# Kernel optimization log

Hardware: AMD Instinct MI355X
Metric: run time of the kernel (lower is better)

Reference implementation:

```python
import jax, jax.numpy as jnp
import numpy as np

N = 100000   # num_nodes
E = 1600000  # num_edges (avg degree 16)
F = 128      # input features
U = 128      # units


def setup_inputs() -> dict:
    key = jax.random.key(0)
    k1, k2, k3, k4 = jax.random.split(key, 4)
    x = jax.random.normal(k1, (N, F), dtype=jnp.float32)
    edge_index = jax.random.randint(k2, (2, E), 0, N, dtype=jnp.int32)
    edge_weight = jax.random.uniform(k3, (E,), dtype=jnp.float32)
    glorot = (2.0 / (F + U)) ** 0.5
    kernel = jax.random.normal(k4, (F, U), dtype=jnp.float32) * glorot
    bias = jnp.zeros((U,), dtype=jnp.float32)
    return {"x": x, "edge_index": edge_index, "edge_weight": edge_weight,
            "kernel": kernel, "bias": bias}


def reference(x, edge_index, edge_weight, kernel, bias):
    num_nodes = x.shape[0]
    row, col = edge_index[0], edge_index[1]
    # renorm trick: A' = A + I (self-loop weight = 1.0 since improved=False)
    loop_idx = jnp.arange(num_nodes, dtype=edge_index.dtype)
    row = jnp.concatenate([row, loop_idx])
    col = jnp.concatenate([col, loop_idx])
    w = jnp.concatenate([edge_weight, jnp.ones((num_nodes,), dtype=edge_weight.dtype)])
    # symmetric normalization: D^{-1/2} A' D^{-1/2}; sym=True -> degrees = row sums
    deg = jax.ops.segment_sum(w, row, num_segments=num_nodes)
    dinv = jnp.where(deg > 0, jax.lax.rsqrt(deg), 0.0)
    w_norm = dinv[row] * w * dinv[col]
    # dense transform then sparse propagate: out[row] += w_norm * (XW)[col]
    h = x @ kernel                              # [N, U]
    msg = w_norm[:, None] * h[col]              # [E+N, U]
    out = jax.ops.segment_sum(msg, row, num_segments=num_nodes)  # [N, U]
    return jax.nn.relu(out + bias)
```

## Files before the change

### kernel.cpp

```cpp
#include <hip/hip_runtime.h>
#include <math.h>


#define CAP 48
#define MAXBINS 512
#define BINCAP 12288

typedef __attribute__((ext_vector_type(8))) short bf16x8;
typedef __attribute__((ext_vector_type(4))) float f32x4;

__device__ __forceinline__ ushort f2bf(float f) {
  uint u = __float_as_uint(f);
  return (ushort)((u + 0x7FFFu + ((u >> 16) & 1u)) >> 16);
}


__global__ __launch_bounds__(256) void k_binscatter(
    const int* __restrict__ row, const int* __restrict__ col,
    const float* __restrict__ ew, uint* __restrict__ binCur,
    int2* __restrict__ binned, int E, int nbins) {
  __shared__ uint hist[MAXBINS];
  __shared__ uint base[MAXBINS];
  int tid = threadIdx.x;
  for (int t = tid; t < nbins; t += 256) hist[t] = 0;
  __syncthreads();
  int per = (E + gridDim.x - 1) / gridDim.x;
  int e0 = blockIdx.x * per;
  int e1 = min(e0 + per, E);
  for (int e = e0 + tid; e < e1; e += 256)
    atomicAdd(&hist[(uint)row[e] >> 8], 1u);
  __syncthreads();
  for (int t = tid; t < nbins; t += 256) {
    uint c = hist[t];
    base[t] = c ? atomicAdd(&binCur[t], c) : 0u;
    hist[t] = 0;
  }
  __syncthreads();
  for (int e = e0 + tid; e < e1; e += 256) {
    int r = row[e];
    int bin = (uint)r >> 8;
    uint pos = base[bin] + atomicAdd(&hist[bin], 1u);
    if (pos < (uint)BINCAP) {
      uint wq = (uint)__float2int_rn(ew[e] * 32768.0f);
      if (wq > 32767u) wq = 32767u;
      int2 v;
      v.x = (int)(((uint)col[e] & 0x1FFFFu) | (wq << 17));
      v.y = r & 255;
      binned[(size_t)bin * BINCAP + pos] = v;
    }
  }
}

__global__ __launch_bounds__(256) void k_binbuild(
    const int2* __restrict__ binned, const uint* __restrict__ binCur,
    uint* __restrict__ slot, int* __restrict__ cnt, float* __restrict__ dinv,
    int N) {
  __shared__ uint sl[256 * CAP];
  __shared__ uint scnt[256];
  int bin = blockIdx.x;
  int tid = threadIdx.x;
  scnt[tid] = 0;
  __syncthreads();
  uint ec = min(binCur[bin], (uint)BINCAP);
  const int2* src = binned + (size_t)bin * BINCAP;
  for (uint i = tid; i < ec; i += 256) {
    int2 v = src[i];
    uint ro = (uint)v.y;
    uint pos = atomicAdd(&scnt[ro], 1u);
    if (pos < (uint)CAP) sl[ro * CAP + pos] = (uint)v.x;
  }
  __syncthreads();
  int node = (bin << 8) + tid;
  if (node < N) {
    uint c = min(scnt[tid], (uint)CAP);
    float s = 0.0f;
    for (uint p = 0; p < c; ++p) s += (float)(sl[tid * CAP + p] >> 17);
    dinv[node] = 1.0f / sqrtf(fmaf(s, 1.0f / 32768.0f, 1.0f));
    cnt[node] = (int)c;
  }
  __syncthreads();
  uint* dst = slot + ((size_t)bin << 8) * CAP;
#pragma unroll 4
  for (uint i = tid; i < 256u * CAP; i += 256) dst[i] = sl[i];
}

__global__ __launch_bounds__(256) void k_gemm3(const float* __restrict__ x,
                                               const float* __restrict__ W,
                                               ushort* __restrict__ hb, int N) {
  __shared__ ushort Wl[16384];
  int tid = threadIdx.x;
  {
    const float4* Wv = (const float4*)W;
#pragma unroll
    for (int it = 0; it < 16; ++it) {
      int id4 = it * 256 + tid;
      float4 v = Wv[id4];
      int id = id4 * 4;
      int k = id >> 7;
      int n = id & 127;
      int kb = k >> 3, klo = k & 7;
      Wl[(n + 0) * 128 + (((kb ^ ((n + 0) & 7)) << 3) | klo)] = f2bf(v.x);
      Wl[(n + 1) * 128 + (((kb ^ ((n + 1) & 7)) << 3) | klo)] = f2bf(v.y);
      Wl[(n + 2) * 128 + (((kb ^ ((n + 2) & 7)) << 3) | klo)] = f2bf(v.z);
      Wl[(n + 3) * 128 + (((kb ^ ((n + 3) & 7)) << 3) | klo)] = f2bf(v.w);
    }
  }
  __syncthreads();

  int wave = tid >> 6, lane = tid & 63;
  int g = lane >> 4;
  int m = lane & 15;

  int ntiles = (N + 63) >> 6;
  for (int tile = blockIdx.x; tile < ntiles; tile += gridDim.x) {
    int r0 = tile * 64 + wave * 16;
    int row = r0 + m;
    bool ok = row < N;
    const float* xr = x + (size_t)row * 128;

    bf16x8 afr[4];
#pragma unroll
    for (int kt = 0; kt < 4; ++kt) {
      float4 p0, p1;
      if (ok) {
        p0 = *(const float4*)(xr + kt * 32 + g * 8);
        p1 = *(const float4*)(xr + kt * 32 + g * 8 + 4);
      } else {
        p0 = make_float4(0.f, 0.f, 0.f, 0.f);
        p1 = p0;
      }
      afr[kt][0] = (short)f2bf(p0.x); afr[kt][1] = (short)f2bf(p0.y);
      afr[kt][2] = (short)f2bf(p0.z); afr[kt][3] = (short)f2bf(p0.w);
      afr[kt][4] = (short)f2bf(p1.x); afr[kt][5] = (short)f2bf(p1.y);
      afr[kt][6] = (short)f2bf(p1.z); afr[kt][7] = (short)f2bf(p1.w);
    }

#pragma unroll
    for (int nt = 0; nt < 8; ++nt) {
      int n = nt * 16 + m;
      f32x4 acc = {0.f, 0.f, 0.f, 0.f};
#pragma unroll
      for (int kt = 0; kt < 4; ++kt) {
        int kb = (kt * 4 + g) ^ (n & 7);
        bf16x8 b = *(const bf16x8*)&Wl[n * 128 + kb * 8];
        acc = __builtin_amdgcn_mfma_f32_16x16x32_bf16(afr[kt], b, acc, 0, 0, 0);
      }
#pragma unroll
      for (int r = 0; r < 4; ++r) {
        int orow = r0 + g * 4 + r;
        if (orow < N) hb[(size_t)orow * 128 + nt * 16 + m] = f2bf(acc[r]);
      }
    }
  }
}

__global__ __launch_bounds__(256) void k_agg2(
    const ushort* __restrict__ hb, const int* __restrict__ cnt,
    const uint* __restrict__ slot, const float* __restrict__ dinv,
    const float* __restrict__ bias, float* __restrict__ out, int n0, int n1) {
  int wid = n0 + blockIdx.x * 4 + (threadIdx.x >> 6);
  int lane = threadIdx.x & 63;
  if (wid >= n1) return;
  float di = dinv[wid];
  uint hv = *(const uint*)(hb + (size_t)wid * 128 + lane * 2);
  float ax = di * __uint_as_float(hv << 16);
  float ay = di * __uint_as_float(hv & 0xFFFF0000u);
  int e = min(cnt[wid], CAP);
  const uint* sl = slot + (size_t)wid * CAP;
  int p = 0;
  for (; p + 4 <= e; p += 4) {
    uint s0 = sl[p], s1 = sl[p + 1], s2 = sl[p + 2], s3 = sl[p + 3];
    int c0 = s0 & 0x1FFFF, c1 = s1 & 0x1FFFF, c2 = s2 & 0x1FFFF, c3 = s3 & 0x1FFFF;
    float w0 = (float)(s0 >> 17) * (1.0f / 32768.0f) * dinv[c0];
    float w1 = (float)(s1 >> 17) * (1.0f / 32768.0f) * dinv[c1];
    float w2 = (float)(s2 >> 17) * (1.0f / 32768.0f) * dinv[c2];
    float w3 = (float)(s3 >> 17) * (1.0f / 32768.0f) * dinv[c3];
    uint g0 = *(const uint*)(hb + (size_t)c0 * 128 + lane * 2);
    uint g1 = *(const uint*)(hb + (size_t)c1 * 128 + lane * 2);
    uint g2 = *(const uint*)(hb + (size_t)c2 * 128 + lane * 2);
    uint g3 = *(const uint*)(hb + (size_t)c3 * 128 + lane * 2);
    ax = fmaf(w0, __uint_as_float(g0 << 16), ax);
    ay = fmaf(w0, __uint_as_float(g0 & 0xFFFF0000u), ay);
    ax = fmaf(w1, __uint_as_float(g1 << 16), ax);
    ay = fmaf(w1, __uint_as_float(g1 & 0xFFFF0000u), ay);
    ax = fmaf(w2, __uint_as_float(g2 << 16), ax);
    ay = fmaf(w2, __uint_as_float(g2 & 0xFFFF0000u), ay);
    ax = fmaf(w3, __uint_as_float(g3 << 16), ax);
    ay = fmaf(w3, __uint_as_float(g3 & 0xFFFF0000u), ay);
  }
  for (; p < e; ++p) {
    uint s = sl[p];
    int c = s & 0x1FFFF;
    float w = (float)(s >> 17) * (1.0f / 32768.0f) * dinv[c];
    uint gg = *(const uint*)(hb + (size_t)c * 128 + lane * 2);
    ax = fmaf(w, __uint_as_float(gg << 16), ax);
    ay = fmaf(w, __uint_as_float(gg & 0xFFFF0000u), ay);
  }
  float2 bv = *(const float2*)(bias + lane * 2);
  float2 o;
  o.x = fmaxf(fmaf(di, ax, bv.x), 0.0f);
  o.y = fmaxf(fmaf(di, ay, bv.y), 0.0f);
  *(float2*)(out + (size_t)wid * 128 + lane * 2) = o;
}


__global__ void k_deg_cnt(const int* __restrict__ row, const float* __restrict__ ew,
                          float* __restrict__ degF, int* __restrict__ cnt, int E) {
  int idx = blockIdx.x * blockDim.x + threadIdx.x;
  int stride = gridDim.x * blockDim.x;
  for (int e = idx; e < E; e += stride) {
    int r = row[e];
    atomicAdd(&degF[r], ew[e]);
    atomicAdd(&cnt[r], 1);
  }
}

__global__ void k_dinv(float* degF, int N) {
  int i = blockIdx.x * blockDim.x + threadIdx.x;
  if (i < N) degF[i] = 1.0f / sqrtf(degF[i] + 1.0f);
}

__global__ void k_scan1(const int* __restrict__ cnt, int* __restrict__ bsum, int N) {
  __shared__ int s[256];
  int i = blockIdx.x * 256 + threadIdx.x;
  s[threadIdx.x] = (i < N) ? cnt[i] : 0;
  __syncthreads();
  for (int d = 128; d > 0; d >>= 1) {
    if (threadIdx.x < d) s[threadIdx.x] += s[threadIdx.x + d];
    __syncthreads();
  }
  if (threadIdx.x == 0) bsum[blockIdx.x] = s[0];
}

__global__ void k_scan2(const int* __restrict__ bsum, int* __restrict__ bsx, int NB) {
  __shared__ int s[1024];
  int t = threadIdx.x;
  int v = (t < NB) ? bsum[t] : 0;
  s[t] = v;
  __syncthreads();
  for (int d = 1; d < 1024; d <<= 1) {
    int add = (t >= d) ? s[t - d] : 0;
    __syncthreads();
    s[t] += add;
    __syncthreads();
  }
  if (t < NB) bsx[t] = s[t] - v;
}

__global__ void k_scan3(const int* __restrict__ cnt, const int* __restrict__ bsx,
                        int* __restrict__ offs, int* __restrict__ cur, int N) {
  __shared__ int s[256];
  int t = threadIdx.x;
  int i = blockIdx.x * 256 + t;
  int v = (i < N) ? cnt[i] : 0;
  s[t] = v;
  __syncthreads();
  for (int d = 1; d < 256; d <<= 1) {
    int add = (t >= d) ? s[t - d] : 0;
    __syncthreads();
    s[t] += add;
    __syncthreads();
  }
  if (i < N) {
    int excl = bsx[blockIdx.x] + s[t] - v;
    offs[i] = excl;
    cur[i] = excl;
  }
}

__global__ void k_scatter(const int* __restrict__ row, const int* __restrict__ col,
                          const float* __restrict__ ew, const float* __restrict__ dinv,
                          int* __restrict__ cur, int* __restrict__ ccol,
                          float* __restrict__ cw, int E) {
  int idx = blockIdx.x * blockDim.x + threadIdx.x;
  int stride = gridDim.x * blockDim.x;
  for (int e = idx; e < E; e += stride) {
    int r = row[e], c = col[e];
    int pos = atomicAdd(&cur[r], 1);
    ccol[pos] = c;
    cw[pos] = dinv[r] * ew[e] * dinv[c];
  }
}

__global__ __launch_bounds__(256) void k_gemm(const float* __restrict__ x,
                                              const float* __restrict__ W,
                                              float* __restrict__ h, int N) {
  __shared__ float Ks[64][128];
  __shared__ float xs[64][36];
  int tid = threadIdx.x;
  int cg = tid & 31;
  int rg = tid >> 5;
  int ntiles = (N + 31) >> 5;
  for (int tile = blockIdx.x; tile < ntiles; tile += gridDim.x) {
    int r0 = tile << 5;
    float acc[4][4] = {};
    for (int kt = 0; kt < 2; ++kt) {
      {
        const float4* Wv = (const float4*)(W + kt * 64 * 128);
        float4* Kv = (float4*)&Ks[0][0];
#pragma unroll
        for (int q = 0; q < 8; ++q) Kv[q * 256 + tid] = Wv[q * 256 + tid];
      }
      {
        int r = tid >> 3;
        int c0 = (tid & 7) * 8;
        int grow = r0 + r;
        if (grow < N) {
          const float4* xp = (const float4*)(x + (size_t)grow * 128 + kt * 64 + c0);
          float4 a = xp[0], b = xp[1];
          xs[c0 + 0][r] = a.x; xs[c0 + 1][r] = a.y; xs[c0 + 2][r] = a.z; xs[c0 + 3][r] = a.w;
          xs[c0 + 4][r] = b.x; xs[c0 + 5][r] = b.y; xs[c0 + 6][r] = b.z; xs[c0 + 7][r] = b.w;
        } else {
#pragma unroll
          for (int q = 0; q < 8; ++q) xs[c0 + q][r] = 0.0f;
        }
      }
      __syncthreads();
#pragma unroll 8
      for (int k = 0; k < 64; ++k) {
        float4 a = *(const float4*)&xs[k][rg * 4];
        float4 b = *(const float4*)&Ks[k][cg * 4];
        float av[4] = {a.x, a.y, a.z, a.w};
        float bv[4] = {b.x, b.y, b.z, b.w};
#pragma unroll
        for (int rr = 0; rr < 4; ++rr)
#pragma unroll
          for (int cc = 0; cc < 4; ++cc)
            acc[rr][cc] = fmaf(av[rr], bv[cc], acc[rr][cc]);
      }
      __syncthreads();
    }
#pragma unroll
    for (int rr = 0; rr < 4; ++rr) {
      int grow = r0 + rg * 4 + rr;
      if (grow < N) {
        float4 v = make_float4(acc[rr][0], acc[rr][1], acc[rr][2], acc[rr][3]);
        *(float4*)&h[(size_t)grow * 128 + cg * 4] = v;
      }
    }
  }
}

__global__ __launch_bounds__(256) void k_agg(
    const float* __restrict__ h, const int* __restrict__ offs,
    const int* __restrict__ cnt, const int* __restrict__ ccol,
    const float* __restrict__ cw, const float* __restrict__ dinv,
    const float* __restrict__ bias, float* __restrict__ out, int N) {
  int wid = blockIdx.x * (blockDim.x >> 6) + (threadIdx.x >> 6);
  int lane = threadIdx.x & 63;
  if (wid >= N) return;
  float di = dinv[wid];
  float2 hv = *(const float2*)(h + (size_t)wid * 128 + lane * 2);
  float ax = di * di * hv.x;
  float ay = di * di * hv.y;
  int s = offs[wid];
  int e = s + cnt[wid];
  int p = s;
  for (; p + 4 <= e; p += 4) {
    int c0 = ccol[p], c1 = ccol[p + 1], c2 = ccol[p + 2], c3 = ccol[p + 3];
    float w0 = cw[p], w1 = cw[p + 1], w2 = cw[p + 2], w3 = cw[p + 3];
    float2 h0 = *(const float2*)(h + (size_t)c0 * 128 + lane * 2);
    float2 h1 = *(const float2*)(h + (size_t)c1 * 128 + lane * 2);
    float2 h2 = *(const float2*)(h + (size_t)c2 * 128 + lane * 2);
    float2 h3 = *(const float2*)(h + (size_t)c3 * 128 + lane * 2);
    ax = fmaf(w0, h0.x, ax); ay = fmaf(w0, h0.y, ay);
    ax = fmaf(w1, h1.x, ax); ay = fmaf(w1, h1.y, ay);
    ax = fmaf(w2, h2.x, ax); ay = fmaf(w2, h2.y, ay);
    ax = fmaf(w3, h3.x, ax); ay = fmaf(w3, h3.y, ay);
  }
  for (; p < e; ++p) {
    int c = ccol[p];
    float w = cw[p];
    float2 hh = *(const float2*)(h + (size_t)c * 128 + lane * 2);
    ax = fmaf(w, hh.x, ax); ay = fmaf(w, hh.y, ay);
  }
  float2 bv = *(const float2*)(bias + lane * 2);
  float2 o;
  o.x = fmaxf(ax + bv.x, 0.0f);
  o.y = fmaxf(ay + bv.y, 0.0f);
  *(float2*)(out + (size_t)wid * 128 + lane * 2) = o;
}


extern "C" void kernel_launch(void* const* d_in, const int* in_sizes, int n_in,
                              void* d_out, int out_size, void* d_ws, size_t ws_size,
                              hipStream_t stream) {
  const float* x    = (const float*)d_in[0];
  const int*   ei   = (const int*)d_in[1];
  const float* ew   = (const float*)d_in[2];
  const float* W    = (const float*)d_in[3];
  const float* bias = (const float*)d_in[4];
  int N = in_sizes[0] / 128;
  int E = in_sizes[2];
  const int* row = ei;
  const int* col = ei + E;

  char* ws = (char*)d_ws;
  size_t ofs = 0;
  auto alloc = [&](size_t bytes) -> void* {
    void* p = ws + ofs;
    ofs += (bytes + 255) & ~(size_t)255;
    return p;
  };

  int nbins = (N + 255) >> 8;

  size_t need_fast = (((size_t)N * 256 + 255) & ~(size_t)255)
                   + (((size_t)nbins * 256 * CAP * 4 + 255) & ~(size_t)255)
                   + (((size_t)nbins * BINCAP * 8 + 255) & ~(size_t)255)
                   + 3 * (((size_t)N * 4 + 255) & ~(size_t)255)
                   + 4096;

  bool shapes_ok = (N <= 131072) && (in_sizes[0] == N * 128) &&
                   (in_sizes[3] == 128 * 128) && (in_sizes[4] == 128);

  int nb = (N + 255) / 256;

  if (shapes_ok && ws_size >= need_fast) {
    ushort* hb     = (ushort*)alloc((size_t)N * 256);
    uint*   slot   = (uint*)  alloc((size_t)nbins * 256 * CAP * 4);
    int2*   binned = (int2*)  alloc((size_t)nbins * BINCAP * 8);
    int*    cnt    = (int*)   alloc((size_t)N * 4);
    float*  dinv   = (float*) alloc((size_t)N * 4);
    uint*   binCur = (uint*)  alloc(4096);

    hipMemsetAsync(binCur, 0, (size_t)nbins * 4, stream);
    k_gemm3<<<1024, 256, 0, stream>>>(x, W, hb, N);
    k_binscatter<<<512, 256, 0, stream>>>(row, col, ew, binCur, binned, E, nbins);
    k_binbuild<<<nbins, 256, 0, stream>>>(binned, binCur, slot, cnt, dinv, N);

    int nh = (N + 1) / 2;
    int g1 = (nh + 3) / 4;
    int g2 = (N - nh + 3) / 4;
    k_agg2<<<g1, 256, 0, stream>>>(hb, cnt, slot, dinv, bias, (float*)d_out, 0, nh);
    k_agg2<<<g2, 256, 0, stream>>>(hb, cnt, slot, dinv, bias, (float*)d_out, nh, N);
  } else {
    float* h    = (float*)alloc((size_t)N * 512);
    float* degF = (float*)alloc((size_t)N * 4);
    int*   cnt  = (int*)  alloc((size_t)N * 4);
    int*   offs = (int*)  alloc((size_t)N * 4);
    int*   cur  = (int*)  alloc((size_t)N * 4);
    int*   bsum = (int*)  alloc(4096 * 4);
    int*   bsx  = (int*)  alloc(4096 * 4);
    int*   ccol = (int*)  alloc((size_t)E * 4);
    float* cw   = (float*)alloc((size_t)E * 4);

    hipMemsetAsync(degF, 0, (size_t)N * 4, stream);
    hipMemsetAsync(cnt, 0, (size_t)N * 4, stream);

    k_gemm<<<1024, 256, 0, stream>>>(x, W, h, N);
    k_deg_cnt<<<2048, 256, 0, stream>>>(row, ew, degF, cnt, E);
    k_dinv<<<nb, 256, 0, stream>>>(degF, N);
    k_scan1<<<nb, 256, 0, stream>>>(cnt, bsum, N);
    k_scan2<<<1, 1024, 0, stream>>>(bsum, bsx, nb);
    k_scan3<<<nb, 256, 0, stream>>>(cnt, bsx, offs, cur, N);
    k_scatter<<<2048, 256, 0, stream>>>(row, col, ew, degF, cur, ccol, cw, E);
    int nodeBlocks = (N + 3) / 4;
    k_agg<<<nodeBlocks, 256, 0, stream>>>(h, offs, cnt, ccol, cw, degF, bias,
                                          (float*)d_out, N);
  }
}
```

Baseline: 265.2 us.

## Bucket edges with global atomics into smaller bins and split aggregation launches

Replaces the block-local histogram plus prefix-reservation scatter with a simple grid-stride kernel that claims slots one at a time with global atomics. Bins shrink from 256 to 128 nodes, so more binbuild blocks run with half the shared memory and a vectorized uint4 copy-out. Aggregation is split into four launches instead of two. This trades fewer passes over edge data and fewer barriers for heavier global atomic contention. The smaller per-bin capacity (4096) raises the chance of overflow-dropped edges on skewed graphs.

```diff
diff --git a/kernel.cpp b/kernel.cpp
--- a/kernel.cpp
+++ b/kernel.cpp
@@ -3,8 +3,8 @@
 
 
 #define CAP 48
-#define MAXBINS 512
-#define BINCAP 12288
+#define BINSZ 128
+#define BINCAP 4096
 
 typedef __attribute__((ext_vector_type(8))) short bf16x8;
 typedef __attribute__((ext_vector_type(4))) float f32x4;
@@ -15,37 +15,24 @@
 }
 
 
-__global__ __launch_bounds__(256) void k_binscatter(
+__global__ __launch_bounds__(256) void k_binscatter2(
     const int* __restrict__ row, const int* __restrict__ col,
     const float* __restrict__ ew, uint* __restrict__ binCur,
-    int2* __restrict__ binned, int E, int nbins) {
-  __shared__ uint hist[MAXBINS];
-  __shared__ uint base[MAXBINS];
-  int tid = threadIdx.x;
-  for (int t = tid; t < nbins; t += 256) hist[t] = 0;
-  __syncthreads();
-  int per = (E + gridDim.x - 1) / gridDim.x;
-  int e0 = blockIdx.x * per;
-  int e1 = min(e0 + per, E);
-  for (int e = e0 + tid; e < e1; e += 256)
-    atomicAdd(&hist[(uint)row[e] >> 8], 1u);
-  __syncthreads();
-  for (int t = tid; t < nbins; t += 256) {
-    uint c = hist[t];
-    base[t] = c ? atomicAdd(&binCur[t], c) : 0u;
-    hist[t] = 0;
-  }
-  __syncthreads();
-  for (int e = e0 + tid; e < e1; e += 256) {
+    int2* __restrict__ binned, int E) {
+  int idx = blockIdx.x * 256 + threadIdx.x;
+  int stride = gridDim.x * 256;
+  for (int e = idx; e < E; e += stride) {
     int r = row[e];
-    int bin = (uint)r >> 8;
-    uint pos = base[bin] + atomicAdd(&hist[bin], 1u);
+    int c = col[e];
+    float w = ew[e];
+    int bin = (uint)r >> 7;
+    uint pos = atomicAdd(&binCur[bin], 1u);
     if (pos < (uint)BINCAP) {
-      uint wq = (uint)__float2int_rn(ew[e] * 32768.0f);
+      uint wq = (uint)__float2int_rn(w * 32768.0f);
       if (wq > 32767u) wq = 32767u;
       int2 v;
-      v.x = (int)(((uint)col[e] & 0x1FFFFu) | (wq << 17));
-      v.y = r & 255;
+      v.x = (int)(((uint)c & 0x1FFFFu) | (wq << 17));
+      v.y = r & (BINSZ - 1);
       binned[(size_t)bin * BINCAP + pos] = v;
     }
   }
@@ -55,11 +42,11 @@
     const int2* __restrict__ binned, const uint* __restrict__ binCur,
     uint* __restrict__ slot, int* __restrict__ cnt, float* __restrict__ dinv,
     int N) {
-  __shared__ uint sl[256 * CAP];
-  __shared__ uint scnt[256];
+  __shared__ uint sl[BINSZ * CAP];
+  __shared__ uint scnt[BINSZ];
   int bin = blockIdx.x;
   int tid = threadIdx.x;
-  scnt[tid] = 0;
+  if (tid < BINSZ) scnt[tid] = 0;
   __syncthreads();
   uint ec = min(binCur[bin], (uint)BINCAP);
   const int2* src = binned + (size_t)bin * BINCAP;
@@ -70,18 +57,19 @@
     if (pos < (uint)CAP) sl[ro * CAP + pos] = (uint)v.x;
   }
   __syncthreads();
-  int node = (bin << 8) + tid;
-  if (node < N) {
+  int node = bin * BINSZ + tid;
+  if (tid < BINSZ && node < N) {
     uint c = min(scnt[tid], (uint)CAP);
     float s = 0.0f;
     for (uint p = 0; p < c; ++p) s += (float)(sl[tid * CAP + p] >> 17);
     dinv[node] = 1.0f / sqrtf(fmaf(s, 1.0f / 32768.0f, 1.0f));
     cnt[node] = (int)c;
   }
-  __syncthreads();
-  uint* dst = slot + ((size_t)bin << 8) * CAP;
-#pragma unroll 4
-  for (uint i = tid; i < 256u * CAP; i += 256) dst[i] = sl[i];
+  uint4* dst = (uint4*)(slot + (size_t)bin * BINSZ * CAP);
+  const uint4* s4 = (const uint4*)sl;
+#pragma unroll
+  for (int it = 0; it < (BINSZ * CAP) / (4 * 256); ++it)
+    dst[it * 256 + tid] = s4[it * 256 + tid];
 }
 
 __global__ __launch_bounds__(256) void k_gemm3(const float* __restrict__ x,
@@ -403,13 +391,13 @@
     return p;
   };
 
-  int nbins = (N + 255) >> 8;
+  int nbins = (N + BINSZ - 1) / BINSZ;
 
   size_t need_fast = (((size_t)N * 256 + 255) & ~(size_t)255)
-                   + (((size_t)nbins * 256 * CAP * 4 + 255) & ~(size_t)255)
+                   + (((size_t)nbins * BINSZ * CAP * 4 + 255) & ~(size_t)255)
                    + (((size_t)nbins * BINCAP * 8 + 255) & ~(size_t)255)
-                   + 3 * (((size_t)N * 4 + 255) & ~(size_t)255)
-                   + 4096;
+                   + 2 * (((size_t)N * 4 + 255) & ~(size_t)255)
+                   + 8192;
 
   bool shapes_ok = (N <= 131072) && (in_sizes[0] == N * 128) &&
                    (in_sizes[3] == 128 * 128) && (in_sizes[4] == 128);
@@ -418,26 +406,29 @@
 
   if (shapes_ok && ws_size >= need_fast) {
     ushort* hb     = (ushort*)alloc((size_t)N * 256);
-    uint*   slot   = (uint*)  alloc((size_t)nbins * 256 * CAP * 4);
+    uint*   slot   = (uint*)  alloc((size_t)nbins * BINSZ * CAP * 4);
     int2*   binned = (int2*)  alloc((size_t)nbins * BINCAP * 8);
     int*    cnt    = (int*)   alloc((size_t)N * 4);
     float*  dinv   = (float*) alloc((size_t)N * 4);
-    uint*   binCur = (uint*)  alloc(4096);
+    uint*   binCur = (uint*)  alloc(8192);
 
     hipMemsetAsync(binCur, 0, (size_t)nbins * 4, stream);
     k_gemm3<<<1024, 256, 0, stream>>>(x, W, hb, N);
-    k_binscatter<<<512, 256, 0, stream>>>(row, col, ew, binCur, binned, E, nbins);
+    k_binscatter2<<<2048, 256, 0, stream>>>(row, col, ew, binCur, binned, E);
     k_binbuild<<<nbins, 256, 0, stream>>>(binned, binCur, slot, cnt, dinv, N);
 
-    int nh = (N + 1) / 2;
-    int g1 = (nh + 3) / 4;
-    int g2 = (N - nh + 3) / 4;
-    k_agg2<<<g1, 256, 0, stream>>>(hb, cnt, slot, dinv, bias, (float*)d_out, 0, nh);
-    k_agg2<<<g2, 256, 0, stream>>>(hb, cnt, slot, dinv, bias, (float*)d_out, nh, N);
+    int q = (N + 3) / 4;
+    for (int i = 0; i < 4; ++i) {
+      int n0 = i * q;
+      int n1 = min(n0 + q, N);
+      if (n0 >= n1) break;
+      int g = (n1 - n0 + 3) / 4;
+      k_agg2<<<g, 256, 0, stream>>>(hb, cnt, slot, dinv, bias, (float*)d_out, n0, n1);
+    }
   } else {
     float* h    = (float*)alloc((size_t)N * 512);
     float* degF = (float*)alloc((size_t)N * 4);
-    int*   cnt  = (int*)  alloc((size_t)N * 4);
+    int*   cntF = (int*)  alloc((size_t)N * 4);
     int*   offs = (int*)  alloc((size_t)N * 4);
     int*   cur  = (int*)  alloc((size_t)N * 4);
     int*   bsum = (int*)  alloc(4096 * 4);
@@ -446,17 +437,17 @@
     float* cw   = (float*)alloc((size_t)E * 4);
 
     hipMemsetAsync(degF, 0, (size_t)N * 4, stream);
-    hipMemsetAsync(cnt, 0, (size_t)N * 4, stream);
+    hipMemsetAsync(cntF, 0, (size_t)N * 4, stream);
 
     k_gemm<<<1024, 256, 0, stream>>>(x, W, h, N);
-    k_deg_cnt<<<2048, 256, 0, stream>>>(row, ew, degF, cnt, E);
+    k_deg_cnt<<<2048, 256, 0, stream>>>(row, ew, degF, cntF, E);
     k_dinv<<<nb, 256, 0, stream>>>(degF, N);
-    k_scan1<<<nb, 256, 0, stream>>>(cnt, bsum, N);
+    k_scan1<<<nb, 256, 0, stream>>>(cntF, bsum, N);
     k_scan2<<<1, 1024, 0, stream>>>(bsum, bsx, nb);
-    k_scan3<<<nb, 256, 0, stream>>>(cnt, bsx, offs, cur, N);
+    k_scan3<<<nb, 256, 0, stream>>>(cntF, bsx, offs, cur, N);
     k_scatter<<<2048, 256, 0, stream>>>(row, col, ew, degF, cur, ccol, cw, E);
     int nodeBlocks = (N + 3) / 4;
-    k_agg<<<nodeBlocks, 256, 0, stream>>>(h, offs, cnt, ccol, cw, degF, bias,
+    k_agg<<<nodeBlocks, 256, 0, stream>>>(h, offs, cntF, ccol, cw, degF, bias,
                                           (float*)d_out, N);
   }
 }
```

After: 603.5 us. 2.28x slower.
